# Kernel optimization log

Measured on AMD Instinct MI355X. Metric: run time of the kernel, lower is better.

The kernel has to match this reference:

```python
import jax, jax.numpy as jnp
import numpy as np
from jax import lax
from jax.scipy.ndimage import map_coordinates

L = 10  # unrolled iterations (LayerNo)


def _conv(x, w, b):
    # x [N,C,H,W], w [O,I,3,3] -> 'SAME' padding == padding=1 for k=3
    y = lax.conv_general_dilated(x, w, (1, 1), 'SAME',
                                 dimension_numbers=('NCHW', 'OIHW', 'NCHW'))
    return y + b[None, :, None, None]


def _prelu(x, a):
    return jnp.where(x >= 0, x, a * x)


def _block(x, w1, b1, a1, w2, b2, a2, w3, b3):
    x = _prelu(_conv(x, w1, b1), a1)
    x = _prelu(_conv(x, w2, b2), a2)
    return _conv(x, w3, b3)


def _radon_forward(img, theta, det_count):
    # img [S,S]; parallel-beam line integrals -> [A, det_count]
    S = img.shape[0]
    c = (S - 1) / 2.0
    s = jnp.arange(det_count, dtype=img.dtype) - (det_count - 1) / 2.0
    t = jnp.arange(S, dtype=img.dtype) - (S - 1) / 2.0

    def one(a):
        ca, sa = jnp.cos(a), jnp.sin(a)
        x = s[:, None] * ca - t[None, :] * sa  # [D,S] sample cols
        y = s[:, None] * sa + t[None, :] * ca  # [D,S] sample rows
        vals = map_coordinates(img, [y + c, x + c], order=1, mode='constant', cval=0.0)
        return vals.sum(axis=1)

    return jax.vmap(one)(theta)


def _radon_backprojection(sino, theta, S):
    # sino [A,D] -> [S,S] (adjoint smear with bilinear detector interpolation)
    A, D = sino.shape
    c = (S - 1) / 2.0
    dc = (D - 1) / 2.0
    ax = jnp.arange(S, dtype=sino.dtype) - c
    Y, X = jnp.meshgrid(ax, ax, indexing='ij')  # row=y, col=x

    def one(row, a):
        ca, sa = jnp.cos(a), jnp.sin(a)
        sidx = (X * ca + Y * sa + dc).ravel()
        return map_coordinates(row, [sidx], order=1, mode='constant', cval=0.0).reshape(S, S)

    return jax.vmap(one)(sino, theta).sum(axis=0)


def _filter_sinogram(sino):
    # Ram-Lak ramp filter along detector axis with FBP normalization pi/(2*A)
    A, D = sino.shape
    n = 2048  # next power of two >= 2*D (D=729)
    F = jnp.fft.rfft(sino, n=n, axis=-1)
    ramp = (2.0 * jnp.fft.rfftfreq(n)).astype(sino.dtype)
    out = jnp.fft.irfft(F * ramp, n=n, axis=-1)[..., :D]
    return out * (jnp.pi / (2.0 * A))


def _forward(cond, x0, g, theta, theta_label,
             dw1, db1, da1, dw2, db2, da2, dw3, db3,
             pw1, pb1, pa1, pw2, pb2, pa2, pw3, pb3):
    S = x0.shape[2]
    A, D = g.shape[2], g.shape[3]
    h = jnp.zeros((1, 5, A, D), dtype=g.dtype)
    f = jnp.zeros((1, 5, S, S), dtype=g.dtype)
    for i in range(L):
        Op_f = _radon_forward(f[0, 1], theta, D)[None, None]          # [1,1,A,D]
        h = h + _block(jnp.concatenate([h, Op_f, g], axis=1),
                       dw1[i], db1[i], da1[i], dw2[i], db2[i], da2[i], dw3[i], db3[i])
        h1 = _filter_sinogram(h[0, 0])                                 # [A,D]
        OpAdj_h = _radon_backprojection(h1, theta, S)[None, None]      # [1,1,S,S]
        f = f + _block(jnp.concatenate([f, OpAdj_h], axis=1),
                       pw1[i], pb1[i], pa1[i], pw2[i], pb2[i], pa2[i], pw3[i], pb3[i])
    return (f[:, 0:1], f[:, 0:1], f[:, 0:1])


def setup_inputs() -> dict:
    key = jax.random.key(0)
    ks = jax.random.split(key, 12)
    S, A, D = 512, 60, 729

    def xavier(k, shp):
        cout, cin = shp[1], shp[2]
        std = np.sqrt(2.0 / ((cin + cout) * 9.0)).astype(np.float32)
        return jax.random.normal(k, shp, dtype=jnp.float32) * std

    ang = jnp.linspace(0.0, np.pi, A, endpoint=False).astype(jnp.float32)
    return {
        'cond': jax.random.normal(ks[0], (1, 1, S, S), dtype=jnp.float32),
        'x0': jax.random.normal(ks[1], (1, 1, S, S), dtype=jnp.float32),
        'g': jax.random.normal(ks[2], (1, 1, A, D), dtype=jnp.float32),
        'theta': ang,
        'theta_label': ang,
        'dw1': xavier(ks[3], (L, 32, 7, 3, 3)), 'db1': jnp.zeros((L, 32), jnp.float32), 'da1': 0.25 * jnp.ones((L,), jnp.float32),
        'dw2': xavier(ks[4], (L, 32, 32, 3, 3)), 'db2': jnp.zeros((L, 32), jnp.float32), 'da2': 0.25 * jnp.ones((L,), jnp.float32),
        'dw3': xavier(ks[5], (L, 5, 32, 3, 3)), 'db3': jnp.zeros((L, 5), jnp.float32),
        'pw1': xavier(ks[6], (L, 32, 6, 3, 3)), 'pb1': jnp.zeros((L, 32), jnp.float32), 'pa1': 0.25 * jnp.ones((L,), jnp.float32),
        'pw2': xavier(ks[7], (L, 32, 32, 3, 3)), 'pb2': jnp.zeros((L, 32), jnp.float32), 'pa2': 0.25 * jnp.ones((L,), jnp.float32),
        'pw3': xavier(ks[8], (L, 5, 32, 3, 3)), 'pb3': jnp.zeros((L, 5), jnp.float32),
    }


def reference(cond, x0, g, theta, theta_label,
              dw1, db1, da1, dw2, db2, da2, dw3, db3,
              pw1, pb1, pa1, pw2, pb2, pa2, pw3, pb3):
    return _forward(cond, x0, g, theta, theta_label,
                    dw1, db1, da1, dw2, db2, da2, dw3, db3,
                    pw1, pb1, pa1, pw2, pb2, pa2, pw3, pb3)
```

## Files before the change

### kernel.cpp

```cpp
#include <hip/hip_runtime.h>
#include <math.h>

#define SS 512
#define AANG 60
#define DDET 729
#define NPIX (SS*SS)
#define NSIN (AANG*DDET)
#define NTAPS 1457
#define DRS 768

typedef float v4u __attribute__((ext_vector_type(4), aligned(4)));
typedef float v4a __attribute__((ext_vector_type(4), aligned(16)));
typedef float v2u __attribute__((ext_vector_type(2), aligned(8)));
typedef float v2a __attribute__((ext_vector_type(2), aligned(4)));
typedef short short8 __attribute__((ext_vector_type(8)));
typedef float f32x4 __attribute__((ext_vector_type(4)));

__device__ inline unsigned short f2bf(float x){
  unsigned u = __float_as_uint(x);
  return (unsigned short)((u + 0x7fffu + ((u >> 16) & 1u)) >> 16);
}

__global__ void trig_kernel(const float* __restrict__ theta, float* __restrict__ trig){
  int a = threadIdx.x;
  if (a < AANG){ trig[a] = cosf(theta[a]); trig[AANG+a] = sinf(theta[a]); }
}

__global__ void taps_kernel(float* __restrict__ taps){
  __shared__ double red[256];
  int m  = blockIdx.x;
  int mm = m - 728;
  double s = 0.0;
  for (int k = 1 + (int)threadIdx.x; k <= 1023; k += 256){
    int phase = (k*mm) & 2047;
    s += (double)k * cos((double)phase * (M_PI/1024.0));
  }
  red[threadIdx.x] = s;
  __syncthreads();
  for (int off=128; off; off>>=1){
    if ((int)threadIdx.x < off) red[threadIdx.x] += red[threadIdx.x+off];
    __syncthreads();
  }
  if (threadIdx.x==0){
    double x = (red[0]*(1.0/512.0) + ((mm & 1) ? -1.0 : 1.0)) / 2048.0;
    taps[m] = (float)(x * (M_PI/120.0));
  }
}

__global__ void transpose_all(const float* __restrict__ s2, float* __restrict__ d2,
                              const float* __restrict__ s5, float* __restrict__ d5){
  int idx = blockIdx.x*256 + (int)threadIdx.x;
  const float* src; float* dst;
  int Cout = 5, Cin = 32;
  if      (idx < 14400){              src=s2; dst=d2; }
  else if (idx < 28800){ idx-=14400;  src=s5; dst=d5; }
  else return;
  int t = idx % 9; int r = idx/9;
  int i = r % Cin; r /= Cin;
  int o = r % Cout; int l = r/Cout;
  dst[((l*Cin+i)*9+t)*Cout+o] = src[idx];
}

__global__ void transpose_w8(const float* __restrict__ src, float* __restrict__ dst, int Cin){
  int idx = blockIdx.x*256 + (int)threadIdx.x;
  int tot = 10*32*Cin*9;
  if (idx >= tot) return;
  int t = idx % 9; int r = idx/9;
  int i = r % Cin; r /= Cin;
  int o = r % 32; int l = r/32;
  int cg = o >> 3, u = o & 7;
  dst[(((l*Cin + i)*4 + cg)*9 + t)*8 + u] = src[idx];
}

__global__ void prep_bimg(const float* __restrict__ w, unsigned short* __restrict__ B){
  int idx = blockIdx.x*256 + (int)threadIdx.x;
  if (idx >= 10*9*2*64*8) return;
  int j    =  idx        & 7;
  int lane = (idx >> 3)  & 63;
  int n    = (idx >> 9)  & 1;
  int r    =  idx >> 10;
  int tap = r % 9, l = r / 9;
  int c = (lane >> 4)*8 + j;
  int o = n*16 + (lane & 15);
  float x = w[(((size_t)(l*32+o)*32 + c)*9) + tap];
  unsigned short hb = f2bf(x);
  float hf = __uint_as_float((unsigned)hb << 16);
  unsigned short lb = f2bf(x - hf);
  size_t d = (size_t)l*18432 + (size_t)tap*2048 + n*1024 + lane*8 + j;
  B[d]       = hb;
  B[d + 512] = lb;
}

__device__ inline void clipr(float al, float ial, float be, float lo, float hi,
                             float& A, float& B, bool& empty){
  if (fabsf(al) < 1e-7f){ if (be < lo || be > hi) empty = true; return; }
  float t0 = (lo - be)*ial, t1 = (hi - be)*ial;
  float mn = fminf(t0,t1), mx = fmaxf(t0,t1);
  A = fmaxf(A, mn); B = fminf(B, mx);
}

__device__ inline float samp_guard(const float* __restrict__ base, float aR, float bR,
                                   float aC, float bC, int t){
  float tp = (float)t - 255.5f;
  float R = fmaf(aR, tp, bR);
  float C = fmaf(aC, tp, bC);
  float rf = floorf(R), cf = floorf(C);
  int r0 = (int)rf, c0 = (int)cf;
  int r1 = r0+1,    c1 = c0+1;
  float fr = R - rf, fc = C - cf;
  bool r0ok = (r0>=0 && r0<SS), r1ok = (r1>=0 && r1<SS);
  bool c0ok = (c0>=0 && c0<SS), c1ok = (c1>=0 && c1<SS);
  float v00 = (r0ok && c0ok) ? base[r0*SS+c0] : 0.f;
  float v01 = (r0ok && c1ok) ? base[r0*SS+c1] : 0.f;
  float v10 = (r1ok && c0ok) ? base[r1*SS+c0] : 0.f;
  float v11 = (r1ok && c1ok) ? base[r1*SS+c1] : 0.f;
  return (1.f-fr)*((1.f-fc)*v00 + fc*v01) + fr*((1.f-fc)*v10 + fc*v11);
}

__global__ __launch_bounds__(256) void radon_fwd_kernel(
    const float* __restrict__ img, const float* __restrict__ imgT,
    const float* __restrict__ trig, float* __restrict__ out){
  int gid  = blockIdx.x*4 + ((int)threadIdx.x >> 6);
  int lane = (int)threadIdx.x & 63;
  if (gid >= NSIN) return;
  int a = gid / DDET;
  int d = gid - a*DDET;
  float ca = trig[a], sa = trig[AANG+a];
  float sd = (float)d - 364.0f;
  float Rc = fmaf(sd, sa, 255.5f);
  float Cc = fmaf(sd, ca, 255.5f);
  float aR = ca, bR = Rc, aC = -sa, bC = Cc;
  const float* base = img;
  if (fabsf(ca) > fabsf(sa)){
    base = imgT;
    float tmp;
    tmp=aR; aR=aC; aC=tmp;
    tmp=bR; bR=bC; bC=tmp;
  }
  float iaR = __builtin_amdgcn_rcpf(aR);
  float iaC = __builtin_amdgcn_rcpf(aC);
  float tiA = -255.5f, tiB = 255.5f;  bool iE=false;
  float teA = -255.5f, teB = 255.5f;  bool eE=false;
  clipr(aR,iaR,bR, 0.001f, 510.999f, tiA,tiB,iE);
  clipr(aC,iaC,bC, 0.001f, 510.999f, tiA,tiB,iE);
  clipr(aR,iaR,bR, -0.999f, 511.999f, teA,teB,eE);
  clipr(aC,iaC,bC, -0.999f, 511.999f, teA,teB,eE);
  float acc = 0.f;
  if (!eE && teA <= teB){
    int eA = max(0,   (int)floorf(teA+255.5f) - 1);
    int eB = min(511, (int)ceilf (teB+255.5f) + 1);
    int iA = (int)ceilf (tiA+255.5f) + 1;
    int iB = (int)floorf(tiB+255.5f) - 1;
    iA = max(iA, eA); iB = min(iB, eB);
    if (iE || iA > iB){
      for (int t = eA+lane; t <= eB; t += 64) acc += samp_guard(base,aR,bR,aC,bC,t);
    } else {
      for (int t = eA+lane;   t <  iA; t += 64) acc += samp_guard(base,aR,bR,aC,bC,t);
      for (int t = iB+1+lane; t <= eB; t += 64) acc += samp_guard(base,aR,bR,aC,bC,t);
      for (int t = iA+lane;   t <= iB; t += 64){
        float tp = (float)t - 255.5f;
        float R = fmaf(aR, tp, bR);
        float C = fmaf(aC, tp, bC);
        int r0 = (int)R, c0 = (int)C;
        float fr = R - (float)r0, fc = C - (float)c0;
        const float* p = base + r0*SS + c0;
        float v00 = p[0], v01 = p[1], v10 = p[SS], v11 = p[SS+1];
        float top = v00 + fc*(v01-v00);
        float bot = v10 + fc*(v11-v10);
        acc += top + fr*(bot-top);
      }
    }
  }
  for (int off=32; off; off>>=1) acc += __shfl_down(acc, off);
  if (lane==0) out[gid] = acc;
}

__global__ __launch_bounds__(256) void filter_kernel2(
    const float* __restrict__ h0, const float* __restrict__ taps,
    float* __restrict__ h1){
  __shared__ float red[256];
  int a  = blockIdx.x / 12;
  int jb = blockIdx.x - a*12;
  int jl = (int)threadIdx.x & 63;
  int kq = (int)threadIdx.x >> 6;
  int j  = jb*64 + jl;
  float acc = 0.f;
  if (j < DDET){
    const float* row = h0 + a*DDET;
    const float* tp  = taps + 728 + j;
    int k0 = kq*183;
    int k1 = min(k0+183, DDET);
    for (int k=k0;k<k1;k++) acc = fmaf(row[k], tp[-k], acc);
  }
  red[threadIdx.x] = acc;
  __syncthreads();
  if ((int)threadIdx.x < 64 && j < DDET){
    float s = red[jl] + red[64+jl] + red[128+jl] + red[192+jl];
    h1[a*DDET + j] = s;
  }
}

__global__ __launch_bounds__(256) void backproj_kernel(
    const float* __restrict__ h1, const float* __restrict__ trig,
    float* __restrict__ out){
  __shared__ float sh[AANG*28];
  __shared__ int   sbase[AANG];
  __shared__ float strig[2*AANG];
  int tid = threadIdx.x;
  int x0 = (blockIdx.x & 31) * 16, y0 = (blockIdx.x >> 5) * 16;
  if (tid < 2*AANG) strig[tid] = trig[tid];
  __syncthreads();
  if (tid < AANG){
    float ca = strig[tid], sa = strig[AANG+tid];
    float Xa = (float)x0 - 255.5f, Xb = Xa + 15.f;
    float Ya = (float)y0 - 255.5f, Yb = Ya + 15.f;
    float s00 = Xa*ca + Ya*sa, s01 = Xb*ca + Ya*sa;
    float s10 = Xa*ca + Yb*sa, s11 = Xb*ca + Yb*sa;
    float mn = fminf(fminf(s00,s01), fminf(s10,s11)) + 364.0f;
    sbase[tid] = (int)floorf(mn) - 2;
  }
  __syncthreads();
  for (int s = tid; s < AANG*28; s += 256){
    int a = s / 28, j = s - a*28;
    int idx = sbase[a] + j;
    sh[s] = (idx >= 0 && idx < DDET) ? h1[a*DDET + idx] : 0.f;
  }
  __syncthreads();
  int x = x0 + (tid & 15), y = y0 + (tid >> 4);
  float X = (float)x - 255.5f, Y = (float)y - 255.5f;
  float acc = 0.f;
  #pragma unroll 6
  for (int a=0;a<AANG;a++){
    float sidx = fmaf(X, strig[a], fmaf(Y, strig[AANG+a], 364.0f));
    float ff = floorf(sidx);
    int k = (int)ff - sbase[a];
    float fi = sidx - ff;
    float v0 = sh[a*28+k], v1 = sh[a*28+k+1];
    acc += v0 + fi*(v1-v0);
  }
  out[y*SS+x] = acc;
}

__global__ __launch_bounds__(256) void conv3x3_dual1(
    const float* __restrict__ in1, int Cin1,
    const float* __restrict__ in2, int Cin2,
    const float* __restrict__ wt,
    const float* __restrict__ bias, const float* __restrict__ prelu,
    unsigned short* __restrict__ outHi, unsigned short* __restrict__ outLo)
{
  const int W = DDET, HW = NSIN;
  int pix = blockIdx.x*256 + (int)threadIdx.x;
  if (pix >= NSIN) return;
  int cg = blockIdx.y;
  int y = pix / W, x = pix - y*W;
  bool ym = y>0, yp = y<AANG-1, xm = x>0, xp = x<W-1;
  float acc[8];
  #pragma unroll
  for (int o=0;o<8;o++) acc[o] = bias[cg*8+o];
  const float* wch = wt + cg*72;
  for (int part=0; part<2; part++){
    const float* src = part ? in2 : in1;
    int nch = part ? Cin2 : Cin1;
    const float* ip = src + pix;
    for (int i=0;i<nch;i++, ip+=HW, wch+=288){
      float p4 = ip[0];
      float p0=0,p1=0,p2=0,p3=0,p5=0,p6=0,p7=0,p8=0;
      if (ym){ p1 = ip[-W]; if (xm) p0 = ip[-W-1]; if (xp) p2 = ip[-W+1]; }
      if (xm) p3 = ip[-1];
      if (xp) p5 = ip[1];
      if (yp){ p7 = ip[W]; if (xm) p6 = ip[W-1]; if (xp) p8 = ip[W+1]; }
      float p[9] = {p0,p1,p2,p3,p4,p5,p6,p7,p8};
      #pragma unroll
      for (int t=0;t<9;t++){
        float v = p[t];
        #pragma unroll
        for (int o=0;o<8;o++) acc[o] = fmaf(v, wch[t*8+o], acc[o]);
      }
    }
  }
  float aa = *prelu;
  short8 vh, vl;
  #pragma unroll
  for (int o=0;o<8;o++){
    float s = acc[o];
    s = (s>=0.f) ? s : aa*s;
    unsigned short hb = f2bf(s);
    float hf = __uint_as_float((unsigned)hb << 16);
    unsigned short lb = f2bf(s - hf);
    vh[o] = (short)hb; vl[o] = (short)lb;
  }
  size_t base = ((size_t)(y+1)*DRS + x)*32 + cg*8;
  *(short8*)(outHi + base) = vh;
  *(short8*)(outLo + base) = vl;
}

__global__ __launch_bounds__(256) void dual_mfma32(
    const unsigned short* __restrict__ hiB, const unsigned short* __restrict__ loB,
    const unsigned short* __restrict__ Bimg,
    const float* __restrict__ bias, const float* __restrict__ prelu,
    float* __restrict__ out)
{
  int y  = blockIdx.y;
  int wv = (int)threadIdx.x >> 6;
  int lane = (int)threadIdx.x & 63;
  int xw = blockIdx.x*256 + wv*64;
  int lm = lane & 15, lq = lane >> 4;
  int laneoff = lm*32 + lq*8;
  f32x4 acc[4][2];
  #pragma unroll
  for (int s=0;s<4;s++){ acc[s][0] = (f32x4)0.f; acc[s][1] = (f32x4)0.f; }
  const short8* Bf = (const short8*)Bimg;
  #pragma unroll
  for (int dy=-1; dy<=1; dy++){
    const unsigned short* rh = hiB + (size_t)(y+dy+1)*DRS*32;
    const unsigned short* rl = loB + (size_t)(y+dy+1)*DRS*32;
    #pragma unroll
    for (int dx=-1; dx<=1; dx++){
      int tap = (dy+1)*3 + (dx+1);
      const short8* bp8 = Bf + tap*256 + lane;
      short8 bh0 = bp8[0];
      short8 bl0 = bp8[64];
      short8 bh1 = bp8[128];
      short8 bl1 = bp8[192];
      int xoff = (xw + dx)*32 + laneoff;
      #pragma unroll
      for (int s=0; s<4; s++){
        short8 ah = *(const short8*)(rh + xoff + s*512);
        short8 al = *(const short8*)(rl + xoff + s*512);
        acc[s][0] = __builtin_amdgcn_mfma_f32_16x16x32_bf16(ah, bh0, acc[s][0], 0,0,0);
        acc[s][1] = __builtin_amdgcn_mfma_f32_16x16x32_bf16(ah, bh1, acc[s][1], 0,0,0);
        acc[s][0] = __builtin_amdgcn_mfma_f32_16x16x32_bf16(al, bh0, acc[s][0], 0,0,0);
        acc[s][1] = __builtin_amdgcn_mfma_f32_16x16x32_bf16(al, bh1, acc[s][1], 0,0,0);
        acc[s][0] = __builtin_amdgcn_mfma_f32_16x16x32_bf16(ah, bl0, acc[s][0], 0,0,0);
        acc[s][1] = __builtin_amdgcn_mfma_f32_16x16x32_bf16(ah, bl1, acc[s][1], 0,0,0);
      }
    }
  }
  float aa = *prelu;
  #pragma unroll
  for (int s=0;s<4;s++){
    int px0 = xw + s*16 + lq*4;
    #pragma unroll
    for (int n=0;n<2;n++){
      int o = n*16 + lm;
      float bv = bias[o];
      f32x4 v = acc[s][n];
      v.x+=bv; v.y+=bv; v.z+=bv; v.w+=bv;
      v.x=(v.x>=0.f)?v.x:aa*v.x; v.y=(v.y>=0.f)?v.y:aa*v.y;
      v.z=(v.z>=0.f)?v.z:aa*v.z; v.w=(v.w>=0.f)?v.w:aa*v.w;
      float* op = out + (size_t)o*NSIN + y*DDET + px0;
      if (px0 + 3 <= DDET-1){
        v4u st; st.x=v.x; st.y=v.y; st.z=v.z; st.w=v.w;
        *(v4u*)op = st;
      } else {
        if (px0   <= DDET-1) op[0] = v.x;
        if (px0+1 <= DDET-1) op[1] = v.y;
        if (px0+2 <= DDET-1) op[2] = v.z;
      }
    }
  }
}

template<int COUT, int W>
__global__ __launch_bounds__(256) void conv3x3_fast2(
    const float* __restrict__ in1, int Cin1,
    const float* __restrict__ wt,
    const float* __restrict__ bias,
    float* __restrict__ out, int H)
{
  __shared__ float red[128*COUT];
  int HW = H*W;
  int pl = (int)threadIdx.x & 127;
  int half = (int)threadIdx.x >> 7;
  int pix = blockIdx.x*128 + pl;
  bool valid = (pix < HW);
  float acc[COUT];
  #pragma unroll
  for (int o=0;o<COUT;o++) acc[o] = 0.f;
  if (valid){
    int y = pix / W, x = pix - y*W;
    bool ym = y>0, yp = y<H-1, xm = x>0, xp = x<W-1;
    int nch = Cin1 >> 1;
    const float* wr = wt + half*nch*9*COUT;
    const float* ip = in1 + pix + (size_t)half*nch*HW;
    for (int i=0;i<nch;i++, ip+=HW){
      float p4 = ip[0];
      float p0=0,p1=0,p2=0,p3=0,p5=0,p6=0,p7=0,p8=0;
      if (ym){ p1 = ip[-W]; if (xm) p0 = ip[-W-1]; if (xp) p2 = ip[-W+1]; }
      if (xm) p3 = ip[-1];
      if (xp) p5 = ip[1];
      if (yp){ p7 = ip[W]; if (xm) p6 = ip[W-1]; if (xp) p8 = ip[W+1]; }
      float p[9] = {p0,p1,p2,p3,p4,p5,p6,p7,p8};
      #pragma unroll
      for (int t=0;t<9;t++){
        float v = p[t];
        #pragma unroll
        for (int o=0;o<COUT;o++) acc[o] = fmaf(v, wr[t*COUT+o], acc[o]);
      }
      wr += 9*COUT;
    }
  }
  if (half == 1){
    #pragma unroll
    for (int o=0;o<COUT;o++) red[pl*COUT+o] = acc[o];
  }
  __syncthreads();
  if (half == 0 && valid){
    float* op = out + pix;
    #pragma unroll
    for (int o=0;o<COUT;o++)
      op[o*HW] += acc[o] + red[pl*COUT+o] + bias[o];
  }
}

__device__ inline void loadrow6(float* R, const float* p, bool valid, bool lE, bool rE){
  if (valid){
    v4u a = *(const v4u*)(p-1);
    v2a b = *(const v2a*)(p+3);
    R[0]=lE?0.f:a.x; R[1]=a.y; R[2]=a.z; R[3]=a.w;
    R[4]=b.x; R[5]=rE?0.f:b.y;
  } else {
    #pragma unroll
    for (int k=0;k<6;k++) R[k]=0.f;
  }
}

__global__ __launch_bounds__(256) void conv3x3_quad6(
    const float* __restrict__ in,
    const float* __restrict__ wt,
    const float* __restrict__ bias, const float* __restrict__ prelu,
    unsigned short* __restrict__ outHi, unsigned short* __restrict__ outLo)
{
  const int W = SS, HW = NPIX;
  int rb = blockIdx.x;
  int cg = blockIdx.y;
  int yb = ((rb & 7) << 5) | (rb >> 3);
  int wv = (int)threadIdx.x >> 6;
  int lane = (int)threadIdx.x & 63;
  int y = yb*2 + (wv >> 1);
  int xb = ((wv & 1) << 8) + lane*4;
  const float* wch = wt + cg*72;
  float acc[4][8];
  #pragma unroll
  for (int px=0;px<4;px++)
    #pragma unroll
    for (int o=0;o<8;o++) acc[px][o] = 0.f;
  bool ym = y>0, yp = y<SS-1;
  bool lE = (xb==0), rE = (xb==508);
  const float* ip = in + y*W + xb;
  for (int i=0;i<6;i++, ip+=HW, wch+=288){
    float R[3][6];
    loadrow6(R[0], ip - W, ym,   lE, rE);
    loadrow6(R[1], ip,     true, lE, rE);
    loadrow6(R[2], ip + W, yp,   lE, rE);
    #pragma unroll
    for (int dy=0;dy<3;dy++){
      #pragma unroll
      for (int dx=0;dx<3;dx++){
        #pragma unroll
        for (int o=0;o<8;o++){
          float w = wch[(dy*3+dx)*8+o];
          #pragma unroll
          for (int px=0;px<4;px++)
            acc[px][o] = fmaf(R[dy][px+dx], w, acc[px][o]);
        }
      }
    }
  }
  float aa = *prelu;
  #pragma unroll
  for (int px=0;px<4;px++){
    short8 vh, vl;
    #pragma unroll
    for (int o=0;o<8;o++){
      float s = acc[px][o] + bias[cg*8+o];
      s = (s>=0.f) ? s : aa*s;
      unsigned short hb = f2bf(s);
      float hf = __uint_as_float((unsigned)hb << 16);
      unsigned short lb = f2bf(s - hf);
      vh[o] = (short)hb; vl[o] = (short)lb;
    }
    size_t base = ((size_t)(y*W + xb + px))*32 + cg*8;
    *(short8*)(outHi + base) = vh;
    *(short8*)(outLo + base) = vl;
  }
}

__global__ __launch_bounds__(256) void conv_mfma32(
    const unsigned short* __restrict__ hiB, const unsigned short* __restrict__ loB,
    const unsigned short* __restrict__ Bimg,
    const float* __restrict__ bias, const float* __restrict__ prelu,
    float* __restrict__ out)
{
  int b = blockIdx.x;
  int by = b >> 1, half = b & 1;
  int y = ((by & 7) << 6) | (by >> 3);
  int wv = (int)threadIdx.x >> 6;
  int lane = (int)threadIdx.x & 63;
  int xw = half*256 + wv*64;
  int lm = lane & 15, lq = lane >> 4;
  int laneoff = lm*32 + lq*8;
  f32x4 acc[4][2];
  #pragma unroll
  for (int s=0;s<4;s++){ acc[s][0] = (f32x4)0.f; acc[s][1] = (f32x4)0.f; }
  bool fastx = (xw != 0) && (xw != 448);
  const short8* Bf = (const short8*)Bimg;
  #pragma unroll
  for (int dy=-1; dy<=1; dy++){
    int yy = y + dy;
    if ((unsigned)yy >= 512u) continue;
    const unsigned short* rh = hiB + (size_t)yy*512*32;
    const unsigned short* rl = loB + (size_t)yy*512*32;
    #pragma unroll
    for (int dx=-1; dx<=1; dx++){
      int tap = (dy+1)*3 + (dx+1);
      const short8* bp8 = Bf + tap*256 + lane;
      short8 bh0 = bp8[0];
      short8 bl0 = bp8[64];
      short8 bh1 = bp8[128];
      short8 bl1 = bp8[192];
      int xoff = (xw + dx)*32 + laneoff;
      #pragma unroll
      for (int s=0; s<4; s++){
        short8 ah, al;
        const unsigned short* ph = rh + xoff + s*512;
        const unsigned short* pl = rl + xoff + s*512;
        if (fastx){
          ah = *(const short8*)ph;
          al = *(const short8*)pl;
        } else {
          int x = xw + s*16 + lm + dx;
          bool ok = ((unsigned)x < 512u);
          ah = ok ? *(const short8*)ph : (short8)0;
          al = ok ? *(const short8*)pl : (short8)0;
        }
        acc[s][0] = __builtin_amdgcn_mfma_f32_16x16x32_bf16(ah, bh0, acc[s][0], 0,0,0);
        acc[s][1] = __builtin_amdgcn_mfma_f32_16x16x32_bf16(ah, bh1, acc[s][1], 0,0,0);
        acc[s][0] = __builtin_amdgcn_mfma_f32_16x16x32_bf16(al, bh0, acc[s][0], 0,0,0);
        acc[s][1] = __builtin_amdgcn_mfma_f32_16x16x32_bf16(al, bh1, acc[s][1], 0,0,0);
        acc[s][0] = __builtin_amdgcn_mfma_f32_16x16x32_bf16(ah, bl0, acc[s][0], 0,0,0);
        acc[s][1] = __builtin_amdgcn_mfma_f32_16x16x32_bf16(ah, bl1, acc[s][1], 0,0,0);
      }
    }
  }
  float aa = *prelu;
  #pragma unroll
  for (int s=0;s<4;s++){
    #pragma unroll
    for (int n=0;n<2;n++){
      int o = n*16 + lm;
      float bv = bias[o];
      f32x4 v = acc[s][n];
      v.x+=bv; v.y+=bv; v.z+=bv; v.w+=bv;
      v.x=(v.x>=0.f)?v.x:aa*v.x; v.y=(v.y>=0.f)?v.y:aa*v.y;
      v.z=(v.z>=0.f)?v.z:aa*v.z; v.w=(v.w>=0.f)?v.w:aa*v.w;
      *(f32x4*)(out + (size_t)o*NPIX + y*SS + xw + s*16 + lq*4) = v;
    }
  }
}

template<int COUT>
__global__ __launch_bounds__(256) void conv3x3_duo(
    const float* __restrict__ in1, int Cin1,
    const float* __restrict__ wt,
    const float* __restrict__ bias,
    float* __restrict__ out,
    float* __restrict__ fout, float* __restrict__ tout)
{
  const int W = SS, HW = NPIX;
  int b = blockIdx.x;
  int y = ((b & 7) << 6) | (b >> 3);
  int x0 = (int)threadIdx.x * 2;
  int pix0 = y*W + x0;
  bool ym = y > 0, yp = y < SS-1;
  bool l0 = x0 > 0;
  bool r3 = x0 + 2 < W;
  float acc0[COUT], acc1[COUT];
  #pragma unroll
  for (int o=0;o<COUT;o++){ float bv = bias[o]; acc0[o]=bv; acc1[o]=bv; }
  const float* wr = wt;
  const float* ip = in1 + pix0;
  #pragma unroll 2
  for (int i=0;i<Cin1;i++, ip+=HW){
    v4u A = ym ? *(const v4u*)(ip - W - 1) : (v4u)0.f;
    v4u B = *(const v4u*)(ip - 1);
    v4u D = yp ? *(const v4u*)(ip + W - 1) : (v4u)0.f;
    if (!l0){ A.x = 0.f; B.x = 0.f; D.x = 0.f; }
    if (!r3){ A.w = 0.f; B.w = 0.f; D.w = 0.f; }
    float w0[9] = {A.x,A.y,A.z, B.x,B.y,B.z, D.x,D.y,D.z};
    float w1[9] = {A.y,A.z,A.w, B.y,B.z,B.w, D.y,D.z,D.w};
    #pragma unroll
    for (int t=0;t<9;t++){
      float v0 = w0[t], v1 = w1[t];
      #pragma unroll
      for (int o=0;o<COUT;o++){
        float w = wr[t*COUT+o];
        acc0[o] = fmaf(v0, w, acc0[o]);
        acc1[o] = fmaf(v1, w, acc1[o]);
      }
    }
    wr += 9*COUT;
  }
  float* op = out + pix0;
  #pragma unroll
  for (int o=0;o<COUT;o++){
    float s0 = acc0[o], s1 = acc1[o];
    v2u old = *(const v2u*)(op + o*HW);
    s0 += old.x; s1 += old.y;
    v2u st; st.x = s0; st.y = s1;
    *(v2u*)(op + o*HW) = st;
    if (o==1 && tout){ tout[x0*SS + y] = s0; tout[(x0+1)*SS + y] = s1; }
    if (o==0 && fout){
      *(v2u*)(fout + pix0) = st;
      *(v2u*)(fout + HW + pix0) = st;
      *(v2u*)(fout + 2*HW + pix0) = st;
    }
  }
}

extern "C" void kernel_launch(void* const* d_in, const int* in_sizes, int n_in,
                              void* d_out, int out_size, void* d_ws, size_t ws_size,
                              hipStream_t stream){
  const float* g     = (const float*)d_in[2];
  const float* theta = (const float*)d_in[3];
  const float* dw1 = (const float*)d_in[5];
  const float* db1 = (const float*)d_in[6];
  const float* da1 = (const float*)d_in[7];
  const float* dw2 = (const float*)d_in[8];
  const float* db2 = (const float*)d_in[9];
  const float* da2 = (const float*)d_in[10];
  const float* dw3 = (const float*)d_in[11];
  const float* db3 = (const float*)d_in[12];
  const float* pw1 = (const float*)d_in[13];
  const float* pb1 = (const float*)d_in[14];
  const float* pa1 = (const float*)d_in[15];
  const float* pw2 = (const float*)d_in[16];
  const float* pb2 = (const float*)d_in[17];
  const float* pa2 = (const float*)d_in[18];
  const float* pw3 = (const float*)d_in[19];
  const float* pb3 = (const float*)d_in[20];

  float* ws     = (float*)d_ws;
  float* trig   = ws;
  float* taps   = ws + 128;
  float* h      = ws + 2048;
  float* opf    = h + 5*NSIN;
  float* gcopy  = opf + NSIN;
  float* h1     = gcopy + NSIN;
  float* f      = h1 + NSIN;
  float* bp     = f + 5*NPIX;
  float* imgT   = bp + NPIX;
  float* dualT1 = imgT + NPIX;
  float* dualT2 = dualT1 + 32*NSIN;
  float* primT2 = dualT2 + 32*NSIN;
  unsigned short* nhwcHi = (unsigned short*)(primT2 + 32*NPIX);
  unsigned short* nhwcLo = nhwcHi + (size_t)32*NPIX;
  float* wsp   = (float*)(nhwcLo + (size_t)32*NPIX);
  float* wtd3  = wsp;
  float* wtp3  = wsp + 14400;
  float* wtd1b = wsp + 28800;
  float* wtd2b = wsp + 48960;
  float* wtp1b = wsp + 141120;
  unsigned short* Bimg  = (unsigned short*)(wsp + 158400);
  unsigned short* Bimg2 = Bimg + 184320;
  const size_t DUALSZ = (size_t)64 + (size_t)62*DRS*32 + 64;
  unsigned short* dualHiRaw = Bimg2 + 184320;
  unsigned short* dualLoRaw = dualHiRaw + DUALSZ;
  unsigned short* dualHi = dualHiRaw + 64;
  unsigned short* dualLo = dualLoRaw + 64;

  hipMemsetAsync(h, 0, (size_t)(5*NSIN)*sizeof(float), stream);
  hipMemsetAsync(f, 0, (size_t)(7*NPIX)*sizeof(float), stream);
  hipMemsetAsync(dualHiRaw, 0, 2*DUALSZ*sizeof(unsigned short), stream);
  hipMemcpyAsync(gcopy, g, (size_t)NSIN*sizeof(float), hipMemcpyDeviceToDevice, stream);
  trig_kernel<<<1,64,0,stream>>>(theta, trig);
  taps_kernel<<<NTAPS,256,0,stream>>>(taps);
  transpose_all<<<(28800+255)/256,256,0,stream>>>(dw3,wtd3, pw3,wtp3);
  transpose_w8<<<(20160+255)/256,256,0,stream>>>(dw1, wtd1b, 7);
  transpose_w8<<<(17280+255)/256,256,0,stream>>>(pw1, wtp1b, 6);
  prep_bimg<<<(92160+255)/256,256,0,stream>>>(pw2, Bimg);
  prep_bimg<<<(92160+255)/256,256,0,stream>>>(dw2, Bimg2);

  const int GD = (NSIN+255)/256;

  for (int i=0;i<10;i++){
    radon_fwd_kernel<<<(NSIN+3)/4,256,0,stream>>>(f + NPIX, imgT, trig, opf);
    conv3x3_dual1<<<dim3(GD,4),256,0,stream>>>(h, 5, opf, 2, wtd1b+(size_t)i*7*288,
                                               db1+(size_t)i*32, da1+i, dualHi, dualLo);
    dual_mfma32<<<dim3(3,AANG),256,0,stream>>>(dualHi, dualLo, Bimg2+(size_t)i*18432,
                                               db2+(size_t)i*32, da2+i, dualT2);
    conv3x3_fast2<5,DDET><<<(NSIN+127)/128,256,0,stream>>>(dualT2, 32, wtd3+i*1440, db3+(size_t)i*5, h, AANG);
    filter_kernel2<<<AANG*12,256,0,stream>>>(h, taps, h1);
    backproj_kernel<<<NPIX/256,256,0,stream>>>(h1, trig, bp);
    conv3x3_quad6<<<dim3(256,4),256,0,stream>>>(f, wtp1b+(size_t)i*6*288, pb1+(size_t)i*32, pa1+i, nhwcHi, nhwcLo);
    conv_mfma32<<<1024,256,0,stream>>>(nhwcHi, nhwcLo, Bimg+(size_t)i*18432, pb2+(size_t)i*32, pa2+i, primT2);
    conv3x3_duo<5><<<SS,256,0,stream>>>(primT2, 32, wtp3+i*1440, pb3+(size_t)i*5, f,
                                        (i==9) ? (float*)d_out : nullptr, imgT);
  }
}
```

Measured before the change: 2.153 ms.

## Run primal third conv on MFMA with split-bf16 NHWC intermediate

The primal conv_mfma32 now writes its 32-channel output as split hi/lo bf16 in NHWC layout, transposed through shared memory, instead of fp32 NCHW. The final 32->5 primal conv, previously a scalar FMA kernel, becomes an MFMA kernel using 3-term split-bf16 products, with weights padded to 16 outputs. This aims to halve the intermediate traffic and move the FMA-heavy third conv onto matrix cores. The cost is MFMA work wasted on zero-padded output channels and the extra shared-memory transpose and sync in conv_mfma32.

```diff
diff --git a/kernel.cpp b/kernel.cpp
--- a/kernel.cpp
+++ b/kernel.cpp
@@ -87,6 +87,24 @@
   float hf = __uint_as_float((unsigned)hb << 16);
   unsigned short lb = f2bf(x - hf);
   size_t d = (size_t)l*18432 + (size_t)tap*2048 + n*1024 + lane*8 + j;
+  B[d]       = hb;
+  B[d + 512] = lb;
+}
+
+__global__ void prep_bimg3(const float* __restrict__ w, unsigned short* __restrict__ B){
+  int idx = blockIdx.x*256 + (int)threadIdx.x;
+  if (idx >= 10*9*64*8) return;
+  int j    =  idx       & 7;
+  int lane = (idx >> 3) & 63;
+  int r    =  idx >> 9;
+  int tap = r % 9, l = r / 9;
+  int c = (lane >> 4)*8 + j;
+  int o = lane & 15;
+  float x = (o < 5) ? w[(((size_t)(l*5+o)*32 + c)*9) + tap] : 0.f;
+  unsigned short hb = f2bf(x);
+  float hf = __uint_as_float((unsigned)hb << 16);
+  unsigned short lb = f2bf(x - hf);
+  size_t d = (size_t)l*9216 + (size_t)tap*1024 + lane*8 + j;
   B[d]       = hb;
   B[d + 512] = lb;
 }
@@ -490,8 +508,9 @@
     const unsigned short* __restrict__ hiB, const unsigned short* __restrict__ loB,
     const unsigned short* __restrict__ Bimg,
     const float* __restrict__ bias, const float* __restrict__ prelu,
-    float* __restrict__ out)
+    unsigned short* __restrict__ outHi, unsigned short* __restrict__ outLo)
 {
+  __shared__ unsigned int tr[4][64][33];
   int b = blockIdx.x;
   int by = b >> 1, half = b & 1;
   int y = ((by & 7) << 6) | (by >> 3);
@@ -554,66 +573,111 @@
       v.x+=bv; v.y+=bv; v.z+=bv; v.w+=bv;
       v.x=(v.x>=0.f)?v.x:aa*v.x; v.y=(v.y>=0.f)?v.y:aa*v.y;
       v.z=(v.z>=0.f)?v.z:aa*v.z; v.w=(v.w>=0.f)?v.w:aa*v.w;
-      *(f32x4*)(out + (size_t)o*NPIX + y*SS + xw + s*16 + lq*4) = v;
-    }
-  }
-}
-
-template<int COUT>
-__global__ __launch_bounds__(256) void conv3x3_duo(
-    const float* __restrict__ in1, int Cin1,
-    const float* __restrict__ wt,
+      #pragma unroll
+      for (int r=0;r<4;r++){
+        float x = v[r];
+        unsigned short hb = f2bf(x);
+        float hf = __uint_as_float((unsigned)hb << 16);
+        unsigned short lb = f2bf(x - hf);
+        tr[wv][s*16 + lq*4 + r][o] = ((unsigned)hb << 16) | (unsigned)lb;
+      }
+    }
+  }
+  __syncthreads();
+  int c8 = lane & 3;
+  int pxl = lane >> 2;
+  #pragma unroll
+  for (int k=0;k<4;k++){
+    int px = pxl + k*16;
+    short8 vh, vl;
+    #pragma unroll
+    for (int j=0;j<8;j++){
+      unsigned p = tr[wv][px][c8*8 + j];
+      vh[j] = (short)(p >> 16);
+      vl[j] = (short)(p & 0xffffu);
+    }
+    size_t base = ((size_t)(y*SS + xw + px))*32 + c8*8;
+    *(short8*)(outHi + base) = vh;
+    *(short8*)(outLo + base) = vl;
+  }
+}
+
+__global__ __launch_bounds__(256) void duo_mfma(
+    const unsigned short* __restrict__ hiB, const unsigned short* __restrict__ loB,
+    const unsigned short* __restrict__ Bimg3,
     const float* __restrict__ bias,
-    float* __restrict__ out,
+    float* __restrict__ f,
     float* __restrict__ fout, float* __restrict__ tout)
 {
-  const int W = SS, HW = NPIX;
   int b = blockIdx.x;
-  int y = ((b & 7) << 6) | (b >> 3);
-  int x0 = (int)threadIdx.x * 2;
-  int pix0 = y*W + x0;
-  bool ym = y > 0, yp = y < SS-1;
-  bool l0 = x0 > 0;
-  bool r3 = x0 + 2 < W;
-  float acc0[COUT], acc1[COUT];
-  #pragma unroll
-  for (int o=0;o<COUT;o++){ float bv = bias[o]; acc0[o]=bv; acc1[o]=bv; }
-  const float* wr = wt;
-  const float* ip = in1 + pix0;
-  #pragma unroll 2
-  for (int i=0;i<Cin1;i++, ip+=HW){
-    v4u A = ym ? *(const v4u*)(ip - W - 1) : (v4u)0.f;
-    v4u B = *(const v4u*)(ip - 1);
-    v4u D = yp ? *(const v4u*)(ip + W - 1) : (v4u)0.f;
-    if (!l0){ A.x = 0.f; B.x = 0.f; D.x = 0.f; }
-    if (!r3){ A.w = 0.f; B.w = 0.f; D.w = 0.f; }
-    float w0[9] = {A.x,A.y,A.z, B.x,B.y,B.z, D.x,D.y,D.z};
-    float w1[9] = {A.y,A.z,A.w, B.y,B.z,B.w, D.y,D.z,D.w};
-    #pragma unroll
-    for (int t=0;t<9;t++){
-      float v0 = w0[t], v1 = w1[t];
+  int by = b >> 1, half = b & 1;
+  int y = ((by & 7) << 6) | (by >> 3);
+  int wv = (int)threadIdx.x >> 6;
+  int lane = (int)threadIdx.x & 63;
+  int xw = half*256 + wv*64;
+  int lm = lane & 15, lq = lane >> 4;
+  int laneoff = lm*32 + lq*8;
+  f32x4 acc[4];
+  #pragma unroll
+  for (int s=0;s<4;s++) acc[s] = (f32x4)0.f;
+  bool fastx = (xw != 0) && (xw != 448);
+  const short8* Bf = (const short8*)Bimg3;
+  #pragma unroll
+  for (int dy=-1; dy<=1; dy++){
+    int yy = y + dy;
+    if ((unsigned)yy >= 512u) continue;
+    const unsigned short* rh = hiB + (size_t)yy*512*32;
+    const unsigned short* rl = loB + (size_t)yy*512*32;
+    #pragma unroll
+    for (int dx=-1; dx<=1; dx++){
+      int tap = (dy+1)*3 + (dx+1);
+      const short8* bp8 = Bf + tap*128 + lane;
+      short8 bh = bp8[0];
+      short8 bl = bp8[64];
+      int xoff = (xw + dx)*32 + laneoff;
       #pragma unroll
-      for (int o=0;o<COUT;o++){
-        float w = wr[t*COUT+o];
-        acc0[o] = fmaf(v0, w, acc0[o]);
-        acc1[o] = fmaf(v1, w, acc1[o]);
-      }
-    }
-    wr += 9*COUT;
-  }
-  float* op = out + pix0;
-  #pragma unroll
-  for (int o=0;o<COUT;o++){
-    float s0 = acc0[o], s1 = acc1[o];
-    v2u old = *(const v2u*)(op + o*HW);
-    s0 += old.x; s1 += old.y;
-    v2u st; st.x = s0; st.y = s1;
-    *(v2u*)(op + o*HW) = st;
-    if (o==1 && tout){ tout[x0*SS + y] = s0; tout[(x0+1)*SS + y] = s1; }
-    if (o==0 && fout){
-      *(v2u*)(fout + pix0) = st;
-      *(v2u*)(fout + HW + pix0) = st;
-      *(v2u*)(fout + 2*HW + pix0) = st;
+      for (int s=0; s<4; s++){
+        short8 ah, al;
+        const unsigned short* ph = rh + xoff + s*512;
+        const unsigned short* pl = rl + xoff + s*512;
+        if (fastx){
+          ah = *(const short8*)ph;
+          al = *(const short8*)pl;
+        } else {
+          int x = xw + s*16 + lm + dx;
+          bool ok = ((unsigned)x < 512u);
+          ah = ok ? *(const short8*)ph : (short8)0;
+          al = ok ? *(const short8*)pl : (short8)0;
+        }
+        acc[s] = __builtin_amdgcn_mfma_f32_16x16x32_bf16(ah, bh, acc[s], 0,0,0);
+        acc[s] = __builtin_amdgcn_mfma_f32_16x16x32_bf16(al, bh, acc[s], 0,0,0);
+        acc[s] = __builtin_amdgcn_mfma_f32_16x16x32_bf16(ah, bl, acc[s], 0,0,0);
+      }
+    }
+  }
+  if (lm < 5){
+    float bv = bias[lm];
+    #pragma unroll
+    for (int s=0;s<4;s++){
+      int px0 = xw + s*16 + lq*4;
+      float* op = f + (size_t)lm*NPIX + y*SS + px0;
+      f32x4 old = *(const f32x4*)op;
+      f32x4 v = acc[s];
+      v.x += old.x + bv; v.y += old.y + bv;
+      v.z += old.z + bv; v.w += old.w + bv;
+      *(f32x4*)op = v;
+      if (lm == 1){
+        tout[(px0  )*SS + y] = v.x;
+        tout[(px0+1)*SS + y] = v.y;
+        tout[(px0+2)*SS + y] = v.z;
+        tout[(px0+3)*SS + y] = v.w;
+      }
+      if (lm == 0 && fout){
+        float* q = fout + y*SS + px0;
+        *(f32x4*)q = v;
+        *(f32x4*)(q + NPIX) = v;
+        *(f32x4*)(q + 2*NPIX) = v;
+      }
     }
   }
 }
@@ -652,8 +716,10 @@
   float* imgT   = bp + NPIX;
   float* dualT1 = imgT + NPIX;
   float* dualT2 = dualT1 + 32*NSIN;
-  float* primT2 = dualT2 + 32*NSIN;
-  unsigned short* nhwcHi = (unsigned short*)(primT2 + 32*NPIX);
+  float* primT2slot = dualT2 + 32*NSIN;
+  unsigned short* primHi = (unsigned short*)primT2slot;
+  unsigned short* primLo = primHi + (size_t)32*NPIX;
+  unsigned short* nhwcHi = (unsigned short*)(primT2slot + 32*NPIX);
   unsigned short* nhwcLo = nhwcHi + (size_t)32*NPIX;
   float* wsp   = (float*)(nhwcLo + (size_t)32*NPIX);
   float* wtd3  = wsp;
@@ -663,8 +729,9 @@
   float* wtp1b = wsp + 141120;
   unsigned short* Bimg  = (unsigned short*)(wsp + 158400);
   unsigned short* Bimg2 = Bimg + 184320;
+  unsigned short* Bimg3 = Bimg2 + 184320;
   const size_t DUALSZ = (size_t)64 + (size_t)62*DRS*32 + 64;
-  unsigned short* dualHiRaw = Bimg2 + 184320;
+  unsigned short* dualHiRaw = Bimg3 + 92160;
   unsigned short* dualLoRaw = dualHiRaw + DUALSZ;
   unsigned short* dualHi = dualHiRaw + 64;
   unsigned short* dualLo = dualLoRaw + 64;
@@ -680,6 +747,7 @@
   transpose_w8<<<(17280+255)/256,256,0,stream>>>(pw1, wtp1b, 6);
   prep_bimg<<<(92160+255)/256,256,0,stream>>>(pw2, Bimg);
   prep_bimg<<<(92160+255)/256,256,0,stream>>>(dw2, Bimg2);
+  prep_bimg3<<<(46080+255)/256,256,0,stream>>>(pw3, Bimg3);
 
   const int GD = (NSIN+255)/256;
 
@@ -693,8 +761,8 @@
     filter_kernel2<<<AANG*12,256,0,stream>>>(h, taps, h1);
     backproj_kernel<<<NPIX/256,256,0,stream>>>(h1, trig, bp);
     conv3x3_quad6<<<dim3(256,4),256,0,stream>>>(f, wtp1b+(size_t)i*6*288, pb1+(size_t)i*32, pa1+i, nhwcHi, nhwcLo);
-    conv_mfma32<<<1024,256,0,stream>>>(nhwcHi, nhwcLo, Bimg+(size_t)i*18432, pb2+(size_t)i*32, pa2+i, primT2);
-    conv3x3_duo<5><<<SS,256,0,stream>>>(primT2, 32, wtp3+i*1440, pb3+(size_t)i*5, f,
-                                        (i==9) ? (float*)d_out : nullptr, imgT);
-  }
-}
+    conv_mfma32<<<1024,256,0,stream>>>(nhwcHi, nhwcLo, Bimg+(size_t)i*18432, pb2+(size_t)i*32, pa2+i, primHi, primLo);
+    duo_mfma<<<1024,256,0,stream>>>(primHi, primLo, Bimg3+(size_t)i*9216, pb3+(size_t)i*5, f,
+                                    (i==9) ? (float*)d_out : nullptr, imgT);
+  }
+}
```

Result: faster. 2.065 ms (-4.1%).
